# Performance work log

Hardware: AMD Instinct MI355X
Metric: run time of the kernel (lower is better)

## Reference

```python
import jax, jax.numpy as jnp
import numpy as np

B, NK, NQ = 16, 1024, 1024
D_IN, D_V, D_H = 3, 8, 128
NUGGET = 1e-3   # diagonal regularizer for the kriging covariance solve
EPS = 1e-12     # keeps sqrt differentiable at zero distance


def _mlp(x, w1, b1, w2, b2, w3, b3):
    # Linear -> ReLU -> Linear -> ReLU -> Linear (torch Linear: y = x @ W.T + b)
    h = jax.nn.relu(x @ w1.T + b1)
    h = jax.nn.relu(h @ w2.T + b2)
    return h @ w3.T + b3


def _cdist(a, b):
    # a: [B,N,D], b: [B,M,D] -> [B,N,M] Euclidean distances
    d2 = (jnp.sum(a * a, -1)[:, :, None]
          + jnp.sum(b * b, -1)[:, None, :]
          - 2.0 * jnp.einsum('bnd,bmd->bnm', a, b))
    return jnp.sqrt(jnp.maximum(d2, 0.0) + EPS)


def _linear_init(key, out_f, in_f):
    k1, k2 = jax.random.split(key)
    lim = 1.0 / np.sqrt(in_f)
    w = jax.random.uniform(k1, (out_f, in_f), jnp.float32, -lim, lim)
    b = jax.random.uniform(k2, (out_f,), jnp.float32, -lim, lim)
    return w, b


def setup_inputs() -> dict:
    key = jax.random.key(0)
    ks = jax.random.split(key, 10)
    KEY = jax.random.normal(ks[0], (B, NK, D_IN), jnp.float32)
    VALUE = jax.random.normal(ks[1], (B, NK, D_V), jnp.float32)
    QUERY = jax.random.normal(ks[2], (B, NQ, D_IN), jnp.float32)
    W1_w, W1_b = _linear_init(ks[3], D_H, D_IN)
    W2_w, W2_b = _linear_init(ks[4], D_H, D_H)
    W3_w, W3_b = _linear_init(ks[5], D_IN, D_H)
    Wv1_w, Wv1_b = _linear_init(ks[6], D_H, D_V)
    Wv2_w, Wv2_b = _linear_init(ks[7], D_H, D_H)
    Wv3_w, Wv3_b = _linear_init(ks[8], D_V, D_H)
    return dict(KEY=KEY, VALUE=VALUE, QUERY=QUERY,
                W1_w=W1_w, W1_b=W1_b, W2_w=W2_w, W2_b=W2_b, W3_w=W3_w, W3_b=W3_b,
                Wv1_w=Wv1_w, Wv1_b=Wv1_b, Wv2_w=Wv2_w, Wv2_b=Wv2_b, Wv3_w=Wv3_w, Wv3_b=Wv3_b)


def reference(KEY, VALUE, QUERY,
              W1_w, W1_b, W2_w, W2_b, W3_w, W3_b,
              Wv1_w, Wv1_b, Wv2_w, Wv2_b, Wv3_w, Wv3_b):
    # shared MLP on KEY and QUERY, separate MLP on VALUE
    Wk = _mlp(KEY, W1_w, W1_b, W2_w, W2_b, W3_w, W3_b)
    Wq = _mlp(QUERY, W1_w, W1_b, W2_w, W2_b, W3_w, W3_b)
    Wv = _mlp(VALUE, Wv1_w, Wv1_b, Wv2_w, Wv2_b, Wv3_w, Wv3_b)
    VALUE_scale = VALUE * Wv                  # einsum('bij,bij->bij')
    # kriging prediction with learned elementwise coordinate scalings
    Ks = KEY * Wk                             # [B,NK,D_IN]
    Qs = QUERY * Wq                           # [B,NQ,D_IN]
    C_kk = jnp.exp(-_cdist(Ks, Ks)) + NUGGET * jnp.eye(NK, dtype=KEY.dtype)  # [B,NK,NK]
    C_qk = jnp.exp(-_cdist(Qs, Ks))                                          # [B,NQ,NK]
    # kriging weights: solve C_kk @ lam = C_qk^T  -> lam [B,NK,NQ]
    lam = jnp.linalg.solve(C_kk, jnp.swapaxes(C_qk, 1, 2))
    # prediction: weighted sum of scaled values -> [B,NQ,D_V]
    return jnp.einsum('bkq,bkv->bqv', lam, VALUE_scale)
```

## Files before the change

kernel.cpp:

```cpp
#include <hip/hip_runtime.h>
#include <hip/hip_bf16.h>


__device__ __forceinline__ int row_of(int e) {
    int i = (int)((sqrtf(8.0f * (float)e + 1.0f) - 1.0f) * 0.5f);
    while ((i + 1) * (i + 2) / 2 <= e) i++;
    while (i * (i + 1) / 2 > e) i--;
    return i;
}

__global__ void k_transpose(const float* __restrict__ W2, const float* __restrict__ Wv2,
                            float* __restrict__ W2T, float* __restrict__ Wv2T) {
    int tid = blockIdx.x * 256 + threadIdx.x;
    int e = tid & 16383;
    int r = e >> 7, c = e & 127;
    if (tid < 16384) W2T[c * 128 + r] = W2[e];
    else             Wv2T[c * 128 + r] = Wv2[e];
}

template<int DI, int P>
__device__ __forceinline__ void mlp_body(const float* __restrict__ in,
                                         float* __restrict__ out, int base,
                                         const float* __restrict__ W1,
                                         const float* __restrict__ b1,
                                         const float* __restrict__ W2T,
                                         const float* __restrict__ b2,
                                         const float* __restrict__ W3,
                                         const float* __restrict__ b3,
                                         float* __restrict__ sh) {
    constexpr int S1 = P + 4;
    float* xs = sh;
    float (*h1T)[S1] = (float(*)[S1])(sh + 128);
    float (*h2)[129] = (float(*)[129])(sh + 128);
    int t = threadIdx.x;
    for (int i = t; i < P * DI; i += 128) xs[i] = in[base * DI + i];
    __syncthreads();
    float w1r[DI];
#pragma unroll
    for (int d = 0; d < DI; d++) w1r[d] = W1[t * DI + d];
    float b1t = b1[t], b2t = b2[t];
    float sp[P];
#pragma unroll
    for (int p = 0; p < P; p++) {
        float s = b1t;
#pragma unroll
        for (int d = 0; d < DI; d++) s += w1r[d] * xs[p * DI + d];
        sp[p] = fmaxf(s, 0.0f);
    }
#pragma unroll
    for (int p4 = 0; p4 < P; p4 += 4)
        *(float4*)&h1T[t][p4] = make_float4(sp[p4], sp[p4 + 1], sp[p4 + 2], sp[p4 + 3]);
    __syncthreads();
    float acc[P];
#pragma unroll
    for (int p = 0; p < P; p++) acc[p] = b2t;
#pragma unroll 4
    for (int k = 0; k < 128; k++) {
        float w = W2T[k * 128 + t];
#pragma unroll
        for (int p4 = 0; p4 < P; p4 += 4) {
            float4 h = *(const float4*)&h1T[k][p4];
            acc[p4    ] += w * h.x;
            acc[p4 + 1] += w * h.y;
            acc[p4 + 2] += w * h.z;
            acc[p4 + 3] += w * h.w;
        }
    }
    __syncthreads();
#pragma unroll
    for (int p = 0; p < P; p++) h2[p][t] = fmaxf(acc[p], 0.0f);
    __syncthreads();
    if (t < P * DI) {
        int p = t / DI, d = t % DI;
        float s = b3[d];
        for (int k = 0; k < 128; k++) s += W3[d * 128 + k] * h2[p][k];
        int gi = base * DI + t;
        out[gi] = in[gi] * s;
    }
}

__global__ __launch_bounds__(128) void k_mlp(
                      const float* __restrict__ KEY, float* __restrict__ Ks,
                      const float* __restrict__ QUERY, float* __restrict__ Qs,
                      const float* __restrict__ VALUE, float* __restrict__ Vs,
                      const float* __restrict__ W1, const float* __restrict__ b1,
                      const float* __restrict__ W2T, const float* __restrict__ b2,
                      const float* __restrict__ W3, const float* __restrict__ b3,
                      const float* __restrict__ Wv1, const float* __restrict__ bv1,
                      const float* __restrict__ Wv2T, const float* __restrict__ bv2,
                      const float* __restrict__ Wv3, const float* __restrict__ bv3) {
    __shared__ __align__(16) float sh[128 + 128 * 36];
    int bx = blockIdx.x;
    if (bx < 512)
        mlp_body<3, 32>(KEY, Ks, bx * 32, W1, b1, W2T, b2, W3, b3, sh);
    else if (bx < 1024)
        mlp_body<3, 32>(QUERY, Qs, (bx - 512) * 32, W1, b1, W2T, b2, W3, b3, sh);
    else
        mlp_body<8, 16>(VALUE, Vs, (bx - 1024) * 16, Wv1, bv1, Wv2T, bv2, Wv3, bv3, sh);
}

__global__ void k_buildC(const float* __restrict__ Ks, float* __restrict__ C) {
    long idx = (long)blockIdx.x * 256 + threadIdx.x;
    int b = (int)(idx >> 20);
    int rem = (int)(idx & 1048575);
    int i = rem >> 10, j = rem & 1023;
    const float* a = Ks + ((long)b * 1024 + i) * 3;
    const float* bb = Ks + ((long)b * 1024 + j) * 3;
    float d0 = a[0] - bb[0], d1 = a[1] - bb[1], d2 = a[2] - bb[2];
    float dist = sqrtf(d0 * d0 + d1 * d1 + d2 * d2 + 1e-12f);
    float v = __expf(-dist);
    if (i == j) v += 1e-3f;
    C[idx] = v;
}

__device__ void potf_body(float* __restrict__ C, float* __restrict__ V,
                          float* smem, int o, int last, int b) {
    int tid = threadIdx.x;
    float* A = C + (long)b * 1048576;
    float* Vp = V + (long)b * 8192;
    float (*T)[132]      = (float(*)[132])smem;
    float (*cv)[8]       = (float(*)[8])(smem + 16896);
    float (*cw)[8]       = (float(*)[8])(smem + 17920);
    float (*Pn)[8]       = (float(*)[8])(smem + 18944);
    float (*St)[32][132] = (float(*)[32][132])(smem + 19968);
    float (*Lc)[32][33]  = (float(*)[32][33])(smem + 19968);
    float* rsd           = smem + 28416;
    float (*Wb)[32][36]  = (float(*)[32][36])(smem + 28544);
    float (*zs)[9]       = (float(*)[9])(smem + 30848);

    bool active = (tid < 272);
    int ti = 0, tj = 0, hh = 0;
    if (active) { int e = tid >> 1; hh = tid & 1; ti = row_of(e); tj = e - ti * (ti + 1) / 2; }
    int r0 = ti * 8 + hh * 4, c0t = tj * 8;
    int lane = tid & 63;
    int sr = tid >> 2, slk = (tid & 3) * 8;

    if (o > 0) {
        const float* sp = A + (long)(o + sr) * 1024 + (o - 128) + slk;
        float4 v0 = *(const float4*)sp;
        float4 v1 = *(const float4*)(sp + 4);
        St[0][slk    ][sr] = v0.x; St[0][slk + 1][sr] = v0.y;
        St[0][slk + 2][sr] = v0.z; St[0][slk + 3][sr] = v0.w;
        St[0][slk + 4][sr] = v1.x; St[0][slk + 5][sr] = v1.y;
        St[0][slk + 6][sr] = v1.z; St[0][slk + 7][sr] = v1.w;
    }
    float Treg[4][8];
    if (active) {
        const float* src = A + (long)(o + r0) * 1024 + o + c0t;
#pragma unroll
        for (int i = 0; i < 4; i++) {
            float4 va = *(const float4*)(src + (long)i * 1024);
            float4 vb = *(const float4*)(src + (long)i * 1024 + 4);
            Treg[i][0] = va.x; Treg[i][1] = va.y; Treg[i][2] = va.z; Treg[i][3] = va.w;
            Treg[i][4] = vb.x; Treg[i][5] = vb.y; Treg[i][6] = vb.z; Treg[i][7] = vb.w;
        }
    }
    if (o > 0) {
        for (int kc = 0; kc < 4; kc++) {
            __syncthreads();
            if (kc < 3) {
                const float* sp = A + (long)(o + sr) * 1024 + (o - 128) + (kc + 1) * 32 + slk;
                float4 v0 = *(const float4*)sp;
                float4 v1 = *(const float4*)(sp + 4);
                int nb = (kc + 1) & 1;
                St[nb][slk    ][sr] = v0.x; St[nb][slk + 1][sr] = v0.y;
                St[nb][slk + 2][sr] = v0.z; St[nb][slk + 3][sr] = v0.w;
                St[nb][slk + 4][sr] = v1.x; St[nb][slk + 5][sr] = v1.y;
                St[nb][slk + 6][sr] = v1.z; St[nb][slk + 7][sr] = v1.w;
            }
            if (active) {
                int buf = kc & 1;
#pragma unroll 4
                for (int k = 0; k < 32; k++) {
                    float4 a0 = *(const float4*)&St[buf][k][r0];
                    float4 b0 = *(const float4*)&St[buf][k][c0t];
                    float4 b1 = *(const float4*)&St[buf][k][c0t + 4];
                    float aa[4] = {a0.x, a0.y, a0.z, a0.w};
                    float bb[8] = {b0.x, b0.y, b0.z, b0.w, b1.x, b1.y, b1.z, b1.w};
#pragma unroll
                    for (int i = 0; i < 4; i++)
#pragma unroll
                        for (int j = 0; j < 8; j++) Treg[i][j] -= aa[i] * bb[j];
                }
            }
        }
    }
    if (active && tj == 0) {
#pragma unroll
        for (int i = 0; i < 4; i++) {
            *(float4*)&Pn[r0 + i][0] = make_float4(Treg[i][0], Treg[i][1], Treg[i][2], Treg[i][3]);
            *(float4*)&Pn[r0 + i][4] = make_float4(Treg[i][4], Treg[i][5], Treg[i][6], Treg[i][7]);
        }
    }
    __syncthreads();
    for (int jbt = 0; jbt < 16; jbt++) {
        int jb = jbt * 8;
        if (tid < 64) {
            int r1 = lane, r2 = 64 + lane;
            float v1[8], v2[8], w1[8], w2[8];
#pragma unroll
            for (int q = 0; q < 8; q++) {
                int j = jb + q;
                int jl = j & 63;
                bool hi = (j >= 64);
                float a1 = Pn[r1][q], a2 = Pn[r2][q];
#pragma unroll
                for (int p = 0; p < 8; p++) {
                    if (p < q) {
                        float wj = __shfl(hi ? w2[p] : w1[p], jl);
                        a1 -= v1[p] * wj;
                        a2 -= v2[p] * wj;
                    }
                }
                v1[q] = a1; v2[q] = a2;
                float dj = __shfl(hi ? a2 : a1, jl);
                float dinv = 1.0f / dj;
                w1[q] = a1 * dinv; w2[q] = a2 * dinv;
            }
            *(float4*)&cv[r1][0] = make_float4(v1[0], v1[1], v1[2], v1[3]);
            *(float4*)&cv[r1][4] = make_float4(v1[4], v1[5], v1[6], v1[7]);
            *(float4*)&cv[r2][0] = make_float4(v2[0], v2[1], v2[2], v2[3]);
            *(float4*)&cv[r2][4] = make_float4(v2[4], v2[5], v2[6], v2[7]);
            *(float4*)&cw[r1][0] = make_float4(w1[0], w1[1], w1[2], w1[3]);
            *(float4*)&cw[r1][4] = make_float4(w1[4], w1[5], w1[6], w1[7]);
            *(float4*)&cw[r2][0] = make_float4(w2[0], w2[1], w2[2], w2[3]);
            *(float4*)&cw[r2][4] = make_float4(w2[4], w2[5], w2[6], w2[7]);
        }
        __syncthreads();
        if (active && tj == jbt) {
#pragma unroll
            for (int i = 0; i < 4; i++) {
                float4 va = *(const float4*)&cv[r0 + i][0];
                float4 vb = *(const float4*)&cv[r0 + i][4];
                Treg[i][0] = va.x; Treg[i][1] = va.y; Treg[i][2] = va.z; Treg[i][3] = va.w;
                Treg[i][4] = vb.x; Treg[i][5] = vb.y; Treg[i][6] = vb.z; Treg[i][7] = vb.w;
            }
        } else if (active && tj > jbt) {
#pragma unroll
            for (int h = 0; h < 2; h++) {
                float va4[4][4], wb4[8][4];
#pragma unroll
                for (int i = 0; i < 4; i++) {
                    float4 v = *(const float4*)&cv[r0 + i][h * 4];
                    va4[i][0] = v.x; va4[i][1] = v.y; va4[i][2] = v.z; va4[i][3] = v.w;
                }
#pragma unroll
                for (int j = 0; j < 8; j++) {
                    float4 v = *(const float4*)&cw[c0t + j][h * 4];
                    wb4[j][0] = v.x; wb4[j][1] = v.y; wb4[j][2] = v.z; wb4[j][3] = v.w;
                }
#pragma unroll
                for (int i = 0; i < 4; i++)
#pragma unroll
                    for (int j = 0; j < 8; j++)
                        Treg[i][j] -= va4[i][0] * wb4[j][0] + va4[i][1] * wb4[j][1]
                                    + va4[i][2] * wb4[j][2] + va4[i][3] * wb4[j][3];
            }
            if (tj == jbt + 1) {
#pragma unroll
                for (int i = 0; i < 4; i++) {
                    *(float4*)&Pn[r0 + i][0] = make_float4(Treg[i][0], Treg[i][1], Treg[i][2], Treg[i][3]);
                    *(float4*)&Pn[r0 + i][4] = make_float4(Treg[i][4], Treg[i][5], Treg[i][6], Treg[i][7]);
                }
            }
        }
        __syncthreads();
    }
    if (active) {
#pragma unroll
        for (int i = 0; i < 4; i++) {
            *(float4*)&T[r0 + i][c0t]     = make_float4(Treg[i][0], Treg[i][1], Treg[i][2], Treg[i][3]);
            *(float4*)&T[r0 + i][c0t + 4] = make_float4(Treg[i][4], Treg[i][5], Treg[i][6], Treg[i][7]);
        }
    }
    __syncthreads();
    if (tid < 128) rsd[tid] = rsqrtf(T[tid][tid]);
    __syncthreads();
    {
        int rg = tid >> 5, cg = tid & 31;
#pragma unroll
        for (int j = 0; j < 4; j++) {
            int c = cg + 32 * j;
#pragma unroll
            for (int i = 0; i < 8; i++) {
                int r = rg * 8 + i;
                if (c <= r) T[r][c] *= rsd[c];
                else        T[r][c] = 0.0f;
            }
        }
    }
    __syncthreads();
    {
        int wv = tid >> 6;
        if (wv < 4 && lane < 32) {
            int d0 = wv * 32;
            int j = lane;
            float x[32];
#pragma unroll
            for (int i = 0; i < 32; i++) {
                float dinv = 1.0f / T[d0 + i][d0 + i];
                float s = 0.0f;
#pragma unroll
                for (int k = 0; k < i; k++) s += T[d0 + i][d0 + k] * x[k];
                x[i] = (i == j) ? dinv : -s * dinv;
            }
#pragma unroll
            for (int i = 0; i < 32; i++) T[d0 + i][d0 + j] = x[i];
        }
        if (tid >= 256) {
            for (int idx = tid - 256; idx < 6144; idx += 256) {
                int p = idx >> 10;
                int e = idx & 1023;
                int r = e >> 5, c = e & 31;
                int i3 = (p == 0) ? 1 : (p <= 2 ? 2 : 3);
                int kb = (p == 0) ? 0 : (p <= 2 ? p - 1 : p - 3);
                Lc[p][r][c] = T[i3 * 32 + r][kb * 32 + c];
            }
        }
    }
    __syncthreads();
    {
        int team = tid >> 8, ttid = tid & 255;
        int orr = ttid >> 3, oc = (ttid & 7) * 4;
        for (int st = 0; st < 3; st++) {
            int i3, j3;
            if (team == 0) { i3 = st + 1; j3 = 0; }
            else           { i3 = (st == 0) ? 2 : 3; j3 = (st == 2) ? 2 : 1; }
            float w0 = 0, w1 = 0, w2 = 0, w3 = 0;
            for (int kb = j3; kb < i3; kb++) {
                int p = i3 * (i3 - 1) / 2 + kb;
#pragma unroll 8
                for (int kk = 0; kk < 32; kk++) {
                    float l = Lc[p][orr][kk];
                    float4 t = *(const float4*)&T[kb * 32 + kk][j3 * 32 + oc];
                    w0 += l * t.x; w1 += l * t.y; w2 += l * t.z; w3 += l * t.w;
                }
            }
            *(float4*)&Wb[team][orr][oc] = make_float4(w0, w1, w2, w3);
            __syncthreads();
            float v0 = 0, v1 = 0, v2 = 0, v3 = 0;
#pragma unroll 8
            for (int kk = 0; kk < 32; kk++) {
                float l = T[i3 * 32 + orr][i3 * 32 + kk];
                float4 wv = *(const float4*)&Wb[team][kk][oc];
                v0 += l * wv.x; v1 += l * wv.y; v2 += l * wv.z; v3 += l * wv.w;
            }
            T[i3 * 32 + orr][j3 * 32 + oc    ] = -v0;
            T[i3 * 32 + orr][j3 * 32 + oc + 1] = -v1;
            T[i3 * 32 + orr][j3 * 32 + oc + 2] = -v2;
            T[i3 * 32 + orr][j3 * 32 + oc + 3] = -v3;
            __syncthreads();
        }
    }
    {
        int r = tid >> 2, c0 = (tid & 3) * 32;
        float* dst = A + (long)(o + r) * 1024 + o + c0;
#pragma unroll
        for (int k = 0; k < 8; k++) {
            int c = c0 + 4 * k;
            *(float4*)(dst + 4 * k) = make_float4(T[r][c], T[r][c + 1], T[r][c + 2], T[r][c + 3]);
        }
    }
    {
        int k = tid >> 2, c2 = (tid & 3) * 2;
        float2 v = *(const float2*)&Vp[(o + k) * 8 + c2];
        zs[k][c2] = v.x; zs[k][c2 + 1] = v.y;
    }
    __syncthreads();
    {
        int r = tid & 127, c2 = (tid >> 7) * 2;
        float y0 = 0, y1 = 0;
#pragma unroll 8
        for (int k = 0; k < 128; k++) {
            float l = T[r][k];
            y0 += l * zs[k][c2];
            y1 += l * zs[k][c2 + 1];
        }
        if (!last) {
            *(float2*)&Vp[(o + r) * 8 + c2] = make_float2(y0, y1);
        } else {
            __syncthreads();
            zs[r][c2] = y0; zs[r][c2 + 1] = y1;
            __syncthreads();
            float x0 = 0, x1 = 0;
#pragma unroll 8
            for (int k = 0; k < 128; k++) {
                float l = T[k][r];
                x0 += l * zs[k][c2];
                x1 += l * zs[k][c2 + 1];
            }
            *(float2*)&Vp[(o + r) * 8 + c2] = make_float2(x0, x1);
        }
    }
}

__device__ void syrk_body(float* __restrict__ C, float* smem,
                          int o, int pti, int ptj, int b) {
    float* A = C + (long)b * 1048576;
    int bi = o + 128 + pti * 128, bj = o + 128 + ptj * 128;
    float (*As)[132] = (float(*)[132])smem;
    float (*Bs)[132] = (float(*)[132])(smem + 4224);
    int tid = threadIdx.x;
    int tx = tid & 15, ty = tid >> 4;
    float acc[4][8] = {};
    int lr = tid >> 2;
    int lk = (tid & 3) * 8;
    bool diag = (bi == bj);
    for (int kc = 0; kc < 128; kc += 32) {
        {
            const float* src = A + (long)(bi + lr) * 1024 + o + kc + lk;
            float4 v0 = *(const float4*)src;
            float4 v1 = *(const float4*)(src + 4);
            As[lk    ][lr] = v0.x; As[lk + 1][lr] = v0.y;
            As[lk + 2][lr] = v0.z; As[lk + 3][lr] = v0.w;
            As[lk + 4][lr] = v1.x; As[lk + 5][lr] = v1.y;
            As[lk + 6][lr] = v1.z; As[lk + 7][lr] = v1.w;
            if (!diag) {
                const float* sb = A + (long)(bj + lr) * 1024 + o + kc + lk;
                float4 w0 = *(const float4*)sb;
                float4 w1 = *(const float4*)(sb + 4);
                Bs[lk    ][lr] = w0.x; Bs[lk + 1][lr] = w0.y;
                Bs[lk + 2][lr] = w0.z; Bs[lk + 3][lr] = w0.w;
                Bs[lk + 4][lr] = w1.x; Bs[lk + 5][lr] = w1.y;
                Bs[lk + 6][lr] = w1.z; Bs[lk + 7][lr] = w1.w;
            }
        }
        __syncthreads();
        {
            float (*Bp)[132] = diag ? As : Bs;
#pragma unroll
            for (int k = 0; k < 32; k++) {
                float4 a0 = *(const float4*)&As[k][ty * 4];
                float4 b0 = *(const float4*)&Bp[k][tx * 8];
                float4 b1 = *(const float4*)&Bp[k][tx * 8 + 4];
                float aa[4] = {a0.x, a0.y, a0.z, a0.w};
                float bb[8] = {b0.x, b0.y, b0.z, b0.w, b1.x, b1.y, b1.z, b1.w};
#pragma unroll
                for (int i = 0; i < 4; i++)
#pragma unroll
                    for (int j = 0; j < 8; j++) acc[i][j] += aa[i] * bb[j];
            }
        }
        __syncthreads();
    }
#pragma unroll
    for (int i = 0; i < 4; i++) {
        int r = bi + ty * 4 + i;
        float* dst = A + (long)r * 1024 + bj + tx * 8;
        if (!diag) {
            float4 p0 = *(const float4*)dst;
            float4 p1 = *(const float4*)(dst + 4);
            p0.x -= acc[i][0]; p0.y -= acc[i][1]; p0.z -= acc[i][2]; p0.w -= acc[i][3];
            p1.x -= acc[i][4]; p1.y -= acc[i][5]; p1.z -= acc[i][6]; p1.w -= acc[i][7];
            *(float4*)dst = p0;
            *(float4*)(dst + 4) = p1;
        } else {
#pragma unroll
            for (int j = 0; j < 8; j++) {
                int c = bj + tx * 8 + j;
                if (c <= r) dst[j] -= acc[i][j];
            }
        }
    }
}

__device__ void zupd_body(const float* __restrict__ C, float* __restrict__ V,
                          float* smem, int o1, int m, int b) {
    const float* A = C + (long)b * 1048576;
    float* Vp = V + (long)b * 8192;
    float (*Lb)[129] = (float(*)[129])smem;
    float (*ys)[9]   = (float(*)[9])(smem + 16512);
    int tid = threadIdx.x;
    int o0 = o1 - 128;
    {
        int kk = tid >> 2, cc = (tid & 3) * 2;
        float2 v = *(const float2*)&Vp[(o0 + kk) * 8 + cc];
        ys[kk][cc] = v.x; ys[kk][cc + 1] = v.y;
    }
#pragma unroll
    for (int mm = 0; mm < 8; mm++) {
        int e = tid + mm * 512;
        int i = e >> 5, j4 = (e & 31) * 4;
        float4 v = *(const float4*)&A[(long)(m * 128 + i) * 1024 + o0 + j4];
        Lb[i][j4] = v.x; Lb[i][j4+1] = v.y; Lb[i][j4+2] = v.z; Lb[i][j4+3] = v.w;
    }
    __syncthreads();
    int r = tid & 127, c2 = (tid >> 7) * 2;
    float u0 = 0, u1 = 0;
#pragma unroll 8
    for (int kk = 0; kk < 128; kk++) {
        float l = Lb[r][kk];
        u0 += l * ys[kk][c2];
        u1 += l * ys[kk][c2 + 1];
    }
    float* vp = &Vp[(m * 128 + r) * 8 + c2];
    float2 old = *(const float2*)vp;
    old.x -= u0; old.y -= u1;
    *(float2*)vp = old;
}

__global__ __launch_bounds__(512) void k_potf_syrk(float* __restrict__ C,
                                                   float* __restrict__ V,
                                                   int o, int last, int nsy) {
    __shared__ __align__(16) float smem[32000];
    int bx = blockIdx.x;
    if (bx < 16) {
        potf_body(C, V, smem, o, last, bx);
    } else if (bx < 16 + nsy) {
        int v = bx - 16;
        int bb = v & 15;
        int p = (v >> 4) + 1;
        int tii = row_of(p);
        int tjj = p - tii * (tii + 1) / 2;
        syrk_body(C, smem, o - 128, tii, tjj, bb);
    } else {
        int v = bx - 16 - nsy;
        int bb = v & 15;
        int zj = v >> 4;
        int m = (o >> 7) + 1 + zj;
        zupd_body(C, V, smem, o, m, bb);
    }
}

__global__ __launch_bounds__(512) void k_trsmg(float* __restrict__ C,
                                               float* __restrict__ V, int o) {
    int b = blockIdx.y;
    float* A = C + (long)b * 1048576;
    float* Vp = V + (long)b * 8192;
    int bi = o + 128 + blockIdx.x * 128;
    const float* Linv = A + (long)o * 1024 + o;
    __shared__ float As[32][132];
    __shared__ float Ls[32][132];
    int tid = threadIdx.x;
    int tx = tid & 15, ty = tid >> 4;
    float acc[4][8] = {};
    int lr = tid >> 2;
    int lk = (tid & 3) * 8;
    for (int kc = 0; kc < 128; kc += 32) {
        {
            const float* src = A + (long)(bi + lr) * 1024 + o + kc + lk;
            const float* sl  = Linv + (long)lr * 1024 + kc + lk;
            float4 v0 = *(const float4*)src;
            float4 v1 = *(const float4*)(src + 4);
            As[lk    ][lr] = v0.x; As[lk + 1][lr] = v0.y;
            As[lk + 2][lr] = v0.z; As[lk + 3][lr] = v0.w;
            As[lk + 4][lr] = v1.x; As[lk + 5][lr] = v1.y;
            As[lk + 6][lr] = v1.z; As[lk + 7][lr] = v1.w;
            float4 w0 = *(const float4*)sl;
            float4 w1 = *(const float4*)(sl + 4);
            Ls[lk    ][lr] = w0.x; Ls[lk + 1][lr] = w0.y;
            Ls[lk + 2][lr] = w0.z; Ls[lk + 3][lr] = w0.w;
            Ls[lk + 4][lr] = w1.x; Ls[lk + 5][lr] = w1.y;
            Ls[lk + 6][lr] = w1.z; Ls[lk + 7][lr] = w1.w;
        }
        __syncthreads();
#pragma unroll
        for (int k = 0; k < 32; k++) {
            float4 a0 = *(const float4*)&As[k][ty * 4];
            float4 b0 = *(const float4*)&Ls[k][tx * 8];
            float4 b1 = *(const float4*)&Ls[k][tx * 8 + 4];
            float aa[4] = {a0.x, a0.y, a0.z, a0.w};
            float bb[8] = {b0.x, b0.y, b0.z, b0.w, b1.x, b1.y, b1.z, b1.w};
#pragma unroll
            for (int i = 0; i < 4; i++)
#pragma unroll
                for (int j = 0; j < 8; j++) acc[i][j] += aa[i] * bb[j];
        }
        __syncthreads();
    }
#pragma unroll
    for (int i = 0; i < 4; i++) {
        float* dst = A + (long)(bi + ty * 4 + i) * 1024 + o + tx * 8;
        *(float4*)dst       = make_float4(acc[i][0], acc[i][1], acc[i][2], acc[i][3]);
        *(float4*)(dst + 4) = make_float4(acc[i][4], acc[i][5], acc[i][6], acc[i][7]);
    }
    if (blockIdx.x != 0) return;
    float* ysf = &Ls[0][0];
    {
        int k = tid >> 2, c2 = (tid & 3) * 2;
        float2 v = *(const float2*)&Vp[(o + k) * 8 + c2];
        ysf[k * 9 + c2] = v.x; ysf[k * 9 + c2 + 1] = v.y;
    }
    __syncthreads();
    float zacc0 = 0, zacc1 = 0;
    int zr = tid & 127, zc0 = (tid >> 7) * 2;
#pragma unroll
    for (int ch = 0; ch < 4; ch++) {
        if ((tx >> 2) == ch) {
            int cb = (tx & 3) * 8;
#pragma unroll
            for (int j = 0; j < 8; j++)
#pragma unroll
                for (int i = 0; i < 4; i++)
                    As[cb + j][ty * 4 + i] = acc[i][j];
        }
        __syncthreads();
#pragma unroll 8
        for (int k = 0; k < 32; k++) {
            float l = As[k][zr];
            const float* yp = &ysf[(ch * 32 + k) * 9 + zc0];
            zacc0 += l * yp[0]; zacc1 += l * yp[1];
        }
        __syncthreads();
    }
    float* vp = &Vp[(bi + zr) * 8 + zc0];
    float2 old = *(const float2*)vp;
    old.x -= zacc0; old.y -= zacc1;
    *(float2*)vp = old;
}

__global__ __launch_bounds__(512) void k_bstep(const float* __restrict__ C,
                                               float* __restrict__ V, int k) {
    int b = blockIdx.y, j = blockIdx.x, tid = threadIdx.x;
    const float* A = C + (long)b * 1048576;
    float* Vp = V + (long)b * 8192;
    __shared__ float Lb[128][129];
    __shared__ float xs[128][9];
    __shared__ float ys[128][9];
    {
        int kk = tid >> 2, c2 = (tid & 3) * 2;
        float2 v = *(const float2*)&Vp[(k * 128 + kk) * 8 + c2];
        xs[kk][c2] = v.x; xs[kk][c2 + 1] = v.y;
    }
#pragma unroll
    for (int m = 0; m < 8; m++) {
        int e = tid + m * 512;
        int i = e >> 5, j4 = (e & 31) * 4;
        float4 v = *(const float4*)&A[(long)(k * 128 + i) * 1024 + j * 128 + j4];
        Lb[i][j4] = v.x; Lb[i][j4+1] = v.y; Lb[i][j4+2] = v.z; Lb[i][j4+3] = v.w;
    }
    __syncthreads();
    int r = tid & 127, c2 = (tid >> 7) * 2;
    float u0 = 0, u1 = 0;
#pragma unroll 8
    for (int kk = 0; kk < 128; kk++) {
        float l = Lb[kk][r];
        u0 += l * xs[kk][c2];
        u1 += l * xs[kk][c2 + 1];
    }
    float* vp = &Vp[(j * 128 + r) * 8 + c2];
    float2 old = *(const float2*)vp;
    old.x -= u0; old.y -= u1;
    if (j < k - 1) {
        *(float2*)vp = old;
    } else {
        ys[r][c2] = old.x; ys[r][c2 + 1] = old.y;
        __syncthreads();
        int o = j * 128;
#pragma unroll
        for (int m = 0; m < 8; m++) {
            int e = tid + m * 512;
            int i = e >> 5, j4 = (e & 31) * 4;
            float4 v = *(const float4*)&A[(long)(o + i) * 1024 + o + j4];
            Lb[i][j4] = v.x; Lb[i][j4+1] = v.y; Lb[i][j4+2] = v.z; Lb[i][j4+3] = v.w;
        }
        __syncthreads();
        float x0 = 0, x1 = 0;
#pragma unroll 8
        for (int kk = 0; kk < 128; kk++) {
            float l = Lb[kk][r];
            x0 += l * ys[kk][c2];
            x1 += l * ys[kk][c2 + 1];
        }
        *(float2*)vp = make_float2(x0, x1);
    }
}

__global__ void k_out(const float* __restrict__ Qs, const float* __restrict__ Ks,
                      const float* __restrict__ X, float* __restrict__ out) {
    int b = blockIdx.x >> 4;
    int qc = blockIdx.x & 15;
    int t = threadIdx.x;
    int q = t & 63, ks = t >> 6;
    __shared__ float kx[1024][3];
    __shared__ __align__(16) float xv[1024][8];
    __shared__ float red[4][64][8];
    for (int i = t; i < 3072; i += 256) kx[i / 3][i % 3] = Ks[b * 3072 + i];
    for (int i = t; i < 8192; i += 256) xv[i >> 3][i & 7] = X[b * 8192 + i];
    __syncthreads();
    int gq = b * 1024 + qc * 64 + q;
    const float* qp = Qs + (long)gq * 3;
    float qx = qp[0], qy = qp[1], qz = qp[2];
    float acc[8] = {};
    int k0 = ks * 256;
#pragma unroll 2
    for (int k = k0; k < k0 + 256; k++) {
        float dx = qx - kx[k][0], dy = qy - kx[k][1], dz = qz - kx[k][2];
        float w = __expf(-sqrtf(dx * dx + dy * dy + dz * dz + 1e-12f));
        float4 xa = *(const float4*)&xv[k][0];
        float4 xb = *(const float4*)&xv[k][4];
        acc[0] += w * xa.x; acc[1] += w * xa.y; acc[2] += w * xa.z; acc[3] += w * xa.w;
        acc[4] += w * xb.x; acc[5] += w * xb.y; acc[6] += w * xb.z; acc[7] += w * xb.w;
    }
#pragma unroll
    for (int c = 0; c < 8; c++) red[ks][q][c] = acc[c];
    __syncthreads();
    if (ks == 0) {
        float* op = out + (long)gq * 8;
#pragma unroll
        for (int c = 0; c < 8; c++)
            op[c] = red[0][q][c] + red[1][q][c] + red[2][q][c] + red[3][q][c];
    }
}

extern "C" void kernel_launch(void* const* d_in, const int* in_sizes, int n_in,
                              void* d_out, int out_size, void* d_ws, size_t ws_size,
                              hipStream_t stream) {
    const float* KEY   = (const float*)d_in[0];
    const float* VALUE = (const float*)d_in[1];
    const float* QUERY = (const float*)d_in[2];
    const float* W1w = (const float*)d_in[3];  const float* W1b = (const float*)d_in[4];
    const float* W2w = (const float*)d_in[5];  const float* W2b = (const float*)d_in[6];
    const float* W3w = (const float*)d_in[7];  const float* W3b = (const float*)d_in[8];
    const float* Wv1w = (const float*)d_in[9]; const float* Wv1b = (const float*)d_in[10];
    const float* Wv2w = (const float*)d_in[11];const float* Wv2b = (const float*)d_in[12];
    const float* Wv3w = (const float*)d_in[13];const float* Wv3b = (const float*)d_in[14];

    float* ws  = (float*)d_ws;
    float* C    = ws;
    float* Ks   = C + 16777216;
    float* Qs   = Ks + 49152;
    float* Vs   = Qs + 49152;
    float* W2T  = Vs + 131072;
    float* Wv2T = W2T + 16384;

    float* out = (float*)d_out;

    hipLaunchKernelGGL(k_transpose, dim3(128), dim3(256), 0, stream, W2w, Wv2w, W2T, Wv2T);
    hipLaunchKernelGGL(k_mlp, dim3(2048), dim3(128), 0, stream,
                       KEY, Ks, QUERY, Qs, VALUE, Vs,
                       W1w, W1b, W2T, W2b, W3w, W3b,
                       Wv1w, Wv1b, Wv2T, Wv2b, Wv3w, Wv3b);
    hipLaunchKernelGGL(k_buildC, dim3(65536), dim3(256), 0, stream, Ks, C);

    for (int s = 0; s < 8; s++) {
        int o = s * 128;
        int np = 0;
        if (s >= 1) { int ntp = 8 - s; np = ntp * (ntp + 1) / 2 - 1; }
        int nz = (s >= 1) ? (7 - s) : 0;
        hipLaunchKernelGGL(k_potf_syrk, dim3(16 + np * 16 + nz * 16), dim3(512), 0, stream,
                           C, Vs, o, (s == 7) ? 1 : 0, np * 16);
        int nt = 7 - s;
        if (nt > 0)
            hipLaunchKernelGGL(k_trsmg, dim3(nt, 16), dim3(512), 0, stream, C, Vs, o);
    }
    for (int k = 7; k >= 1; k--)
        hipLaunchKernelGGL(k_bstep, dim3(k, 16), dim3(512), 0, stream, C, Vs, k);

    hipLaunchKernelGGL(k_out, dim3(256), dim3(256), 0, stream, Qs, Ks, Vs, out);
}
```

Baseline: 954.8 us.

## Fuse covariance build into first Cholesky step and overlap it with panel factorization

Removes the standalone covariance-building kernel. At step zero the 16 factorization blocks compute their diagonal 128x128 tile straight from the scaled keys in shared memory, and 240 extra rider blocks fill the rest of C with a grid-stride loop. This saves one launch and lets the C build run alongside the first panel factorization. The risk is that only 256 blocks now write about 64 MB of C, which may lower memory-level parallelism compared with 65536 blocks, and step zero becomes a longer critical path.

```diff
diff --git a/kernel.cpp b/kernel.cpp
--- a/kernel.cpp
+++ b/kernel.cpp
@@ -99,21 +99,27 @@
         mlp_body<8, 16>(VALUE, Vs, (bx - 1024) * 16, Wv1, bv1, Wv2T, bv2, Wv3, bv3, sh);
 }
 
-__global__ void k_buildC(const float* __restrict__ Ks, float* __restrict__ C) {
-    long idx = (long)blockIdx.x * 256 + threadIdx.x;
-    int b = (int)(idx >> 20);
-    int rem = (int)(idx & 1048575);
-    int i = rem >> 10, j = rem & 1023;
-    const float* a = Ks + ((long)b * 1024 + i) * 3;
-    const float* bb = Ks + ((long)b * 1024 + j) * 3;
-    float d0 = a[0] - bb[0], d1 = a[1] - bb[1], d2 = a[2] - bb[2];
-    float dist = sqrtf(d0 * d0 + d1 * d1 + d2 * d2 + 1e-12f);
-    float v = __expf(-dist);
-    if (i == j) v += 1e-3f;
-    C[idx] = v;
+__device__ void buildc_rider(const float* __restrict__ Ks, float* __restrict__ C,
+                             int rid, int nrid) {
+    const long total = 16777216;
+    long stride = (long)nrid * 512;
+    for (long idx = (long)rid * 512 + threadIdx.x; idx < total; idx += stride) {
+        int b = (int)(idx >> 20);
+        int rem = (int)(idx & 1048575);
+        int i = rem >> 10, j = rem & 1023;
+        if (i < 128 && j < 128) continue;
+        const float* a = Ks + ((long)b * 1024 + i) * 3;
+        const float* bb = Ks + ((long)b * 1024 + j) * 3;
+        float d0 = a[0] - bb[0], d1 = a[1] - bb[1], d2 = a[2] - bb[2];
+        float dist = sqrtf(d0 * d0 + d1 * d1 + d2 * d2 + 1e-12f);
+        float v = __expf(-dist);
+        if (i == j) v += 1e-3f;
+        C[idx] = v;
+    }
 }
 
 __device__ void potf_body(float* __restrict__ C, float* __restrict__ V,
+                          const float* __restrict__ KsD,
                           float* smem, int o, int last, int b) {
     int tid = threadIdx.x;
     float* A = C + (long)b * 1048576;
@@ -127,6 +133,7 @@
     float* rsd           = smem + 28416;
     float (*Wb)[32][36]  = (float(*)[32][36])(smem + 28544);
     float (*zs)[9]       = (float(*)[9])(smem + 30848);
+    float* kxs           = smem + 19968;
 
     bool active = (tid < 272);
     int ti = 0, tj = 0, hh = 0;
@@ -145,7 +152,26 @@
         St[0][slk + 6][sr] = v1.z; St[0][slk + 7][sr] = v1.w;
     }
     float Treg[4][8];
-    if (active) {
+    if (o == 0) {
+        for (int i = tid; i < 384; i += 512) kxs[i] = KsD[(long)b * 3072 + i];
+        __syncthreads();
+        if (active) {
+#pragma unroll
+            for (int i = 0; i < 4; i++) {
+#pragma unroll
+                for (int j = 0; j < 8; j++) {
+                    int r = r0 + i, c = c0t + j;
+                    float d0 = kxs[r * 3    ] - kxs[c * 3    ];
+                    float d1 = kxs[r * 3 + 1] - kxs[c * 3 + 1];
+                    float d2 = kxs[r * 3 + 2] - kxs[c * 3 + 2];
+                    float dist = sqrtf(d0 * d0 + d1 * d1 + d2 * d2 + 1e-12f);
+                    float v = __expf(-dist);
+                    if (r == c) v += 1e-3f;
+                    Treg[i][j] = v;
+                }
+            }
+        }
+    } else if (active) {
         const float* src = A + (long)(o + r0) * 1024 + o + c0t;
 #pragma unroll
         for (int i = 0; i < 4; i++) {
@@ -501,11 +527,14 @@
 
 __global__ __launch_bounds__(512) void k_potf_syrk(float* __restrict__ C,
                                                    float* __restrict__ V,
+                                                   const float* __restrict__ Ks,
                                                    int o, int last, int nsy) {
     __shared__ __align__(16) float smem[32000];
     int bx = blockIdx.x;
     if (bx < 16) {
-        potf_body(C, V, smem, o, last, bx);
+        potf_body(C, V, Ks, smem, o, last, bx);
+    } else if (o == 0) {
+        buildc_rider(Ks, C, bx - 16, gridDim.x - 16);
     } else if (bx < 16 + nsy) {
         int v = bx - 16;
         int bb = v & 15;
@@ -731,15 +760,15 @@
                        KEY, Ks, QUERY, Qs, VALUE, Vs,
                        W1w, W1b, W2T, W2b, W3w, W3b,
                        Wv1w, Wv1b, Wv2T, Wv2b, Wv3w, Wv3b);
-    hipLaunchKernelGGL(k_buildC, dim3(65536), dim3(256), 0, stream, Ks, C);
 
     for (int s = 0; s < 8; s++) {
         int o = s * 128;
         int np = 0;
         if (s >= 1) { int ntp = 8 - s; np = ntp * (ntp + 1) / 2 - 1; }
         int nz = (s >= 1) ? (7 - s) : 0;
-        hipLaunchKernelGGL(k_potf_syrk, dim3(16 + np * 16 + nz * 16), dim3(512), 0, stream,
-                           C, Vs, o, (s == 7) ? 1 : 0, np * 16);
+        int nrid = (s == 0) ? 240 : 0;
+        hipLaunchKernelGGL(k_potf_syrk, dim3(16 + np * 16 + nz * 16 + nrid), dim3(512), 0, stream,
+                           C, Vs, Ks, o, (s == 7) ? 1 : 0, np * 16);
         int nt = 7 - s;
         if (nt > 0)
             hipLaunchKernelGGL(k_trsmg, dim3(nt, 16), dim3(512), 0, stream, C, Vs, o);
```

New measurement: 939.2 us (median of 2 runs). Within noise of the previous version (-1.6%).
